# Kernel tuning notes

Measured on AMD Instinct MI355X. Metric: run time of the kernel, lower is better.

The kernel has to match this reference:

```python
import jax, jax.numpy as jnp
import numpy as np

DIM_GATE = 256
DIM_BIAS = 128
H = 8
D = 32
EPS = 1e-5


def _layernorm(t, gamma, beta):
    mu = jnp.mean(t, axis=-1, keepdims=True)
    var = jnp.mean(jnp.square(t - mu), axis=-1, keepdims=True)
    return (t - mu) * jax.lax.rsqrt(var + EPS) * gamma + beta


def setup_inputs() -> dict:
    key = jax.random.key(0)
    ks = jax.random.split(key, 12)
    b, l = 2, 512
    x = jax.random.normal(ks[0], (b, l, DIM_GATE), dtype=jnp.float32)
    bias = jax.random.normal(ks[1], (b, l, l, DIM_BIAS), dtype=jnp.float32)
    s_g = 1.0 / np.sqrt(DIM_GATE)
    s_b = 1.0 / np.sqrt(DIM_BIAS)
    return {
        "x": x,
        "bias": bias,
        "g_gamma": jnp.ones((DIM_GATE,), jnp.float32),
        "g_beta": jnp.zeros((DIM_GATE,), jnp.float32),
        "b_gamma": jnp.ones((DIM_BIAS,), jnp.float32),
        "b_beta": jnp.zeros((DIM_BIAS,), jnp.float32),
        "Wq": jax.random.normal(ks[2], (DIM_GATE, H * D), jnp.float32) * s_g,
        "Wk": jax.random.normal(ks[3], (DIM_GATE, H * D), jnp.float32) * s_g,
        "Wv": jax.random.normal(ks[4], (DIM_GATE, H * D), jnp.float32) * s_g,
        "Wb": jax.random.normal(ks[5], (DIM_BIAS, H), jnp.float32) * s_b,
        "Wg": jax.random.normal(ks[6], (DIM_GATE, H * D), jnp.float32) * s_g,
        "bg": jnp.zeros((H * D,), jnp.float32),
        "Wout": jax.random.normal(ks[7], (H * D, DIM_GATE), jnp.float32) * s_g,
        "bout": jnp.zeros((DIM_GATE,), jnp.float32),
    }


def reference(x, bias, g_gamma, g_beta, b_gamma, b_beta, Wq, Wk, Wv, Wb, Wg, bg, Wout, bout):
    b, l, _ = x.shape
    scaling = 1.0 / np.sqrt(D)
    xn = _layernorm(x, g_gamma, g_beta)                      # [b,l,dg]
    bn = _layernorm(bias, b_gamma, b_beta)                   # [b,l,l,db]
    q = (xn @ Wq).reshape(b, l, H, D)                        # [b,l,h,d]
    k = (xn @ Wk).reshape(b, l, H, D) * scaling
    v = (xn @ Wv).reshape(b, l, H, D)
    pair_b = bn @ Wb                                         # [b,q,k,h]
    gate = jax.nn.sigmoid(xn @ Wg + bg)                      # [b,l,h*d]
    attn = jnp.einsum('bqhd,bkhd->bqkh', q, k) + pair_b      # [b,q,k,h]
    attn = jax.nn.softmax(attn, axis=-2)                     # softmax over k
    out = jnp.einsum('bqkh,bkhd->bqhd', attn, v).reshape(b, l, H * D)
    out = gate * out
    return out @ Wout + bout
```

## Files before the change

### kernel.cpp

```cpp
#include <hip/hip_runtime.h>
#include <math.h>

#define LSEQ 512
#define DG 256
#define DB 128
#define NH 8
#define HD 32
#define EPSV 1e-5f
#define LP2 516

typedef __attribute__((ext_vector_type(8))) short bf16x8;
typedef __attribute__((ext_vector_type(4))) float f32x4;

__device__ __forceinline__ unsigned short f2bf(float x) {
    unsigned int u = __float_as_uint(x);
    u += 0x7FFFu + ((u >> 16) & 1u);
    return (unsigned short)(u >> 16);
}
__device__ __forceinline__ float bf2f(unsigned short h) {
    return __uint_as_float(((unsigned int)h) << 16);
}

__global__ __launch_bounds__(256) void prep_pairb_kernel(
    const float* __restrict__ x, const float* __restrict__ g_gamma,
    const float* __restrict__ g_beta, const float* __restrict__ Wq,
    const float* __restrict__ Wk, const float* __restrict__ Wv,
    const float* __restrict__ Wg, const float* __restrict__ bg,
    float* __restrict__ q_ws, float* __restrict__ k_ws,
    float* __restrict__ v_ws, float* __restrict__ g_ws,
    const float* __restrict__ bias, const float* __restrict__ b_gamma,
    const float* __restrict__ b_beta, const float* __restrict__ Wb,
    float* __restrict__ pair_ws)
{
    __shared__ float lds[4 * 2 * 2048];
    const int t = threadIdx.x;

    if (blockIdx.x < 256) {
        float (*xs)[DG] = (float(*)[DG])lds;
        const int wave = t >> 6, lane = t & 63;
        const int row0 = blockIdx.x << 2;

        {
            const int row = row0 + wave;
            const float4 xv = *(const float4*)(x + (size_t)row * DG + lane * 4);
            float s  = xv.x + xv.y + xv.z + xv.w;
            float ss = xv.x*xv.x + xv.y*xv.y + xv.z*xv.z + xv.w*xv.w;
            #pragma unroll
            for (int m = 32; m >= 1; m >>= 1) { s += __shfl_xor(s, m); ss += __shfl_xor(ss, m); }
            const float mean = s * (1.f / DG);
            const float rstd = rsqrtf(ss * (1.f / DG) - mean * mean + EPSV);
            const float4 gg = *(const float4*)(g_gamma + lane * 4);
            const float4 gb = *(const float4*)(g_beta + lane * 4);
            float4 xo;
            xo.x = (xv.x - mean) * rstd * gg.x + gb.x;
            xo.y = (xv.y - mean) * rstd * gg.y + gb.y;
            xo.z = (xv.z - mean) * rstd * gg.z + gb.z;
            xo.w = (xv.w - mean) * rstd * gg.w + gb.w;
            *(float4*)&xs[wave][lane * 4] = xo;
        }
        __syncthreads();

        float aq[4] = {0,0,0,0}, ak[4] = {0,0,0,0}, av[4] = {0,0,0,0}, ag[4] = {0,0,0,0};
        #pragma unroll 4
        for (int c = 0; c < DG; ++c) {
            const float wq = Wq[(size_t)c * DG + t];
            const float wk = Wk[(size_t)c * DG + t];
            const float wv = Wv[(size_t)c * DG + t];
            const float wg = Wg[(size_t)c * DG + t];
            #pragma unroll
            for (int r = 0; r < 4; ++r) {
                const float xr = xs[r][c];
                aq[r] = fmaf(xr, wq, aq[r]);
                ak[r] = fmaf(xr, wk, ak[r]);
                av[r] = fmaf(xr, wv, av[r]);
                ag[r] = fmaf(xr, wg, ag[r]);
            }
        }

        const float scal = 0.17677669529663687f;
        const float bgv = bg[t];
        #pragma unroll
        for (int r = 0; r < 4; ++r) {
            const size_t o = (size_t)(row0 + r) * DG + t;
            q_ws[o] = aq[r];
            k_ws[o] = ak[r] * scal;
            v_ws[o] = av[r];
            g_ws[o] = 1.f / (1.f + __expf(-(ag[r] + bgv)));
        }
        return;
    }

    const int w = t >> 6, l = t & 63;
    const int n = l & 15, quad = l >> 4;
    const int bq = blockIdx.x - 256;

    bf16x8 gwhi[4], gwlo[4];
    float S1 = 0.f, S0 = 0.f;
    #pragma unroll
    for (int ks = 0; ks < 4; ++ks) {
        #pragma unroll
        for (int j = 0; j < 8; ++j) {
            const int c = ks * 32 + quad * 8 + j;
            const float wb = (n < 8) ? Wb[c * 8 + n] : 0.f;
            const float wv = b_gamma[c] * wb;
            S1 += wv;
            S0 += b_beta[c] * wb;
            unsigned short hi = f2bf(wv);
            unsigned short lo = f2bf(wv - bf2f(hi));
            if (n == 8) { hi = 0x3F80; lo = 0; }
            gwhi[ks][j] = (short)hi;
            gwlo[ks][j] = (short)lo;
        }
    }
    S1 += __shfl_xor(S1, 16); S1 += __shfl_xor(S1, 32);
    S0 += __shfl_xor(S0, 16); S0 += __shfl_xor(S0, 32);

    float* myl = lds + w * 4096;
    const size_t rowbase = (size_t)bq * LSEQ + w * 16;

    auto stage = [&](int tt, int buf) {
        const float* src = bias + (rowbase + (size_t)tt * 64) * DB;
        float* dst = myl + buf * 2048;
        #pragma unroll
        for (int i = 0; i < 8; ++i) {
            __builtin_amdgcn_global_load_lds(
                (const __attribute__((address_space(1))) void*)(src + i * 256 + l * 4),
                (__attribute__((address_space(3))) void*)(dst + i * 256 + l * 4),
                16, 0, 0);
        }
    };

    auto compute = [&](int tt, int buf) {
        const float* d = myl + buf * 2048 + n * 128 + quad * 8;
        f32x4 acc = {0.f, 0.f, 0.f, 0.f};
        float ssq = 0.f;
        #pragma unroll
        for (int ks = 0; ks < 4; ++ks) {
            const float4 x0 = *(const float4*)(d + ks * 32);
            const float4 x1 = *(const float4*)(d + ks * 32 + 4);
            ssq = fmaf(x0.x,x0.x, fmaf(x0.y,x0.y, fmaf(x0.z,x0.z, fmaf(x0.w,x0.w, ssq))));
            ssq = fmaf(x1.x,x1.x, fmaf(x1.y,x1.y, fmaf(x1.z,x1.z, fmaf(x1.w,x1.w, ssq))));
            const float xsv[8] = {x0.x,x0.y,x0.z,x0.w,x1.x,x1.y,x1.z,x1.w};
            bf16x8 ahi, alo;
            #pragma unroll
            for (int j = 0; j < 8; ++j) {
                const unsigned short hi = f2bf(xsv[j]);
                ahi[j] = (short)hi;
                alo[j] = (short)f2bf(xsv[j] - bf2f(hi));
            }
            acc = __builtin_amdgcn_mfma_f32_16x16x32_bf16(ahi, gwhi[ks], acc, 0, 0, 0);
            acc = __builtin_amdgcn_mfma_f32_16x16x32_bf16(alo, gwhi[ks], acc, 0, 0, 0);
            acc = __builtin_amdgcn_mfma_f32_16x16x32_bf16(ahi, gwlo[ks], acc, 0, 0, 0);
        }
        ssq += __shfl_xor(ssq, 16);
        ssq += __shfl_xor(ssq, 32);
        float* pout = pair_ws + (rowbase + (size_t)tt * 64 + quad * 4) * NH + n;
        #pragma unroll
        for (int reg = 0; reg < 4; ++reg) {
            const float sumr = __uint_as_float((unsigned)__builtin_amdgcn_ds_bpermute(
                (quad * 16 + 8) * 4, (int)__float_as_uint(acc[reg])));
            const float ssqr = __uint_as_float((unsigned)__builtin_amdgcn_ds_bpermute(
                (quad * 4 + reg) * 4, (int)__float_as_uint(ssq)));
            const float mean = sumr * (1.f / DB);
            const float var  = ssqr * (1.f / DB) - mean * mean;
            const float rstd = rsqrtf(var + EPSV);
            const float p = rstd * (acc[reg] - mean * S1) + S0;
            if (n < NH) pout[reg * NH] = p;
        }
    };

    stage(0, 0);
    stage(1, 1);
    asm volatile("s_waitcnt vmcnt(8)" ::: "memory");
    compute(0, 0);
    for (int tt = 1; tt < 7; ++tt) {
        stage(tt + 1, (tt + 1) & 1);
        asm volatile("s_waitcnt vmcnt(12)" ::: "memory");
        compute(tt, tt & 1);
    }
    asm volatile("s_waitcnt vmcnt(4)" ::: "memory");
    compute(7, 1);
}

__global__ __launch_bounds__(512) void attn_kernel(
    const float* __restrict__ pair_ws, const float* __restrict__ Wout,
    const float* __restrict__ bout, const float* __restrict__ q_ws,
    const float* __restrict__ k_ws, const float* __restrict__ v_ws,
    const float* __restrict__ g_ws, float* __restrict__ out)
{
    __shared__ float lg[2 * NH * LP2];
    __shared__ float q_s[2 * DG];
    __shared__ float ps[4 * 2 * 64 * 4];
    __shared__ float row_s[2 * DG];
    __shared__ float rden[16];

    const int t = threadIdx.x;
    const int b = blockIdx.x >> 8;
    const int q0 = (blockIdx.x & 255) * 2;

    {
        const float* pbase = pair_ws + ((size_t)(b * LSEQ + q0)) * LSEQ * NH;
        #pragma unroll
        for (int r = 0; r < 4; ++r) {
            const int f = r * 512 + t;
            const float4 pv = *(const float4*)(pbase + (size_t)f * 4);
            const int q = f >> 10;
            const int o = (f * 4) & 4095;
            const int k = o >> 3, hb = o & 7;
            float* dst = lg + (q * NH + hb) * LP2 + k;
            dst[0] = pv.x; dst[LP2] = pv.y; dst[2*LP2] = pv.z; dst[3*LP2] = pv.w;
        }
        q_s[t] = q_ws[((size_t)(b * LSEQ + q0)) * DG + t];
    }
    __syncthreads();

    {
        const int h = t >> 6;
        const int lane = t & 63;
        const int d4 = lane >> 3, r = lane & 7;
        const float4 qa = *(const float4*)(q_s + h * HD + d4 * 4);
        const float4 qb = *(const float4*)(q_s + DG + h * HD + d4 * 4);
        const float* kbase = k_ws + ((size_t)(b * LSEQ)) * DG + h * HD + d4 * 4;
        float* l0 = lg + (0 * NH + h) * LP2;
        float* l1 = lg + (1 * NH + h) * LP2;
        #pragma unroll 4
        for (int kb8 = 0; kb8 < 64; ++kb8) {
            const int krow = kb8 * 8 + r;
            const float4 kv = *(const float4*)(kbase + (size_t)krow * DG);
            float a0 = fmaf(kv.x, qa.x, fmaf(kv.y, qa.y, fmaf(kv.z, qa.z, kv.w * qa.w)));
            float a1 = fmaf(kv.x, qb.x, fmaf(kv.y, qb.y, fmaf(kv.z, qb.z, kv.w * qb.w)));
            a0 += __shfl_xor(a0, 8);  a1 += __shfl_xor(a1, 8);
            a0 += __shfl_xor(a0, 16); a1 += __shfl_xor(a1, 16);
            a0 += __shfl_xor(a0, 32); a1 += __shfl_xor(a1, 32);
            if (d4 == 0) { l0[krow] += a0; l1[krow] += a1; }
        }
    }
    __syncthreads();

    {
        const int qh = t >> 5, l32 = t & 31;
        float* lrow = lg + qh * LP2;
        float mx = -1e30f;
        #pragma unroll
        for (int i = 0; i < 16; ++i) mx = fmaxf(mx, lrow[l32 + i * 32]);
        #pragma unroll
        for (int m = 16; m >= 1; m >>= 1) mx = fmaxf(mx, __shfl_xor(mx, m));
        float s = 0.f;
        #pragma unroll
        for (int i = 0; i < 16; ++i) {
            const int k = l32 + i * 32;
            const float e = __expf(lrow[k] - mx);
            lrow[k] = e;
            s += e;
        }
        #pragma unroll
        for (int m = 16; m >= 1; m >>= 1) s += __shfl_xor(s, m);
        if (l32 == 0) rden[qh] = 1.f / s;
    }
    __syncthreads();

    {
        const int q = t >> 8, s4 = (t >> 6) & 3, c4 = t & 63;
        const int h = c4 >> 3;
        const float* vb = v_ws + ((size_t)(b * LSEQ + s4 * 128)) * DG + c4 * 4;
        const float* prow = lg + (q * NH + h) * LP2 + s4 * 128;
        float4 a = {0.f, 0.f, 0.f, 0.f};
        #pragma unroll 4
        for (int i = 0; i < 128; ++i) {
            const float p = prow[i];
            const float4 vv = *(const float4*)(vb + (size_t)i * DG);
            a.x = fmaf(p, vv.x, a.x);
            a.y = fmaf(p, vv.y, a.y);
            a.z = fmaf(p, vv.z, a.z);
            a.w = fmaf(p, vv.w, a.w);
        }
        *(float4*)&ps[((s4 * 2 + q) * 64 + c4) * 4] = a;
    }
    __syncthreads();
    if (t < 128) {
        const int q = t >> 6, c4 = t & 63, h = c4 >> 3;
        float4 a = *(const float4*)&ps[((0 * 2 + q) * 64 + c4) * 4];
        #pragma unroll
        for (int s4 = 1; s4 < 4; ++s4) {
            const float4 p4 = *(const float4*)&ps[((s4 * 2 + q) * 64 + c4) * 4];
            a.x += p4.x; a.y += p4.y; a.z += p4.z; a.w += p4.w;
        }
        const float sc = rden[q * NH + h];
        const float4 g4 = *(const float4*)(g_ws + ((size_t)(b * LSEQ + q0 + q)) * DG + c4 * 4);
        float* rs = row_s + q * DG + c4 * 4;
        rs[0] = a.x * sc * g4.x;
        rs[1] = a.y * sc * g4.y;
        rs[2] = a.z * sc * g4.z;
        rs[3] = a.w * sc * g4.w;
    }
    __syncthreads();

    {
        const int q = t >> 8, co = t & 255;
        const float* rs = row_s + q * DG;
        const float* wo = Wout + co;
        float a = 0.f;
        #pragma unroll 4
        for (int c = 0; c < DG; ++c)
            a = fmaf(rs[c], wo[(size_t)c * DG], a);
        out[((size_t)(b * LSEQ + q0 + q)) * DG + co] = a + bout[co];
    }
}

extern "C" void kernel_launch(void* const* d_in, const int* in_sizes, int n_in,
                              void* d_out, int out_size, void* d_ws, size_t ws_size,
                              hipStream_t stream)
{
    const float* x       = (const float*)d_in[0];
    const float* bias    = (const float*)d_in[1];
    const float* g_gamma = (const float*)d_in[2];
    const float* g_beta  = (const float*)d_in[3];
    const float* b_gamma = (const float*)d_in[4];
    const float* b_beta  = (const float*)d_in[5];
    const float* Wq      = (const float*)d_in[6];
    const float* Wk      = (const float*)d_in[7];
    const float* Wv      = (const float*)d_in[8];
    const float* Wb      = (const float*)d_in[9];
    const float* Wg      = (const float*)d_in[10];
    const float* bg      = (const float*)d_in[11];
    const float* Wout    = (const float*)d_in[12];
    const float* bout    = (const float*)d_in[13];
    float* out = (float*)d_out;

    float* ws      = (float*)d_ws;
    float* q_ws    = ws;
    float* k_ws    = ws + 262144;
    float* v_ws    = ws + 2 * 262144;
    float* g_ws    = ws + 3 * 262144;
    float* pair_ws = ws + 4 * 262144;

    hipLaunchKernelGGL(prep_pairb_kernel, dim3(1280), dim3(256), 0, stream,
                       x, g_gamma, g_beta, Wq, Wk, Wv, Wg, bg,
                       q_ws, k_ws, v_ws, g_ws,
                       bias, b_gamma, b_beta, Wb, pair_ws);
    hipLaunchKernelGGL(attn_kernel, dim3(512), dim3(512), 0, stream,
                       pair_ws, Wout, bout, q_ws, k_ws, v_ws, g_ws, out);
}
```

Baseline: 473.3 us.

## Fuse pair-bias layernorm projection into attention kernel, one query row per block

Moves the pair-bias layernorm+projection out of the prep kernel and into the attention kernel, so each block computes its query row's bias logits directly into LDS instead of writing them to and reading them back from a global workspace. Bias staging grows to triple buffering and is issued before the QK dot products, so the bias loads overlap that work. The attention kernel now handles one query row per 256-thread block (1024 blocks) instead of two rows per 512-thread block. The trade-off is that the QK^T, PV and output projection work no longer shares K, V and Wout loads across two queries, and LDS use per block rises, which may lower occupancy.

```diff
diff --git a/kernel.cpp b/kernel.cpp
--- a/kernel.cpp
+++ b/kernel.cpp
@@ -21,78 +21,87 @@
     return __uint_as_float(((unsigned int)h) << 16);
 }
 
-__global__ __launch_bounds__(256) void prep_pairb_kernel(
+__global__ __launch_bounds__(256) void prep_kernel(
     const float* __restrict__ x, const float* __restrict__ g_gamma,
     const float* __restrict__ g_beta, const float* __restrict__ Wq,
     const float* __restrict__ Wk, const float* __restrict__ Wv,
     const float* __restrict__ Wg, const float* __restrict__ bg,
     float* __restrict__ q_ws, float* __restrict__ k_ws,
-    float* __restrict__ v_ws, float* __restrict__ g_ws,
+    float* __restrict__ v_ws, float* __restrict__ g_ws)
+{
+    __shared__ float xs[4][DG];
+    const int t = threadIdx.x;
+    const int wave = t >> 6, lane = t & 63;
+    const int row0 = blockIdx.x << 2;
+
+    {
+        const int row = row0 + wave;
+        const float4 xv = *(const float4*)(x + (size_t)row * DG + lane * 4);
+        float s  = xv.x + xv.y + xv.z + xv.w;
+        float ss = xv.x*xv.x + xv.y*xv.y + xv.z*xv.z + xv.w*xv.w;
+        #pragma unroll
+        for (int m = 32; m >= 1; m >>= 1) { s += __shfl_xor(s, m); ss += __shfl_xor(ss, m); }
+        const float mean = s * (1.f / DG);
+        const float rstd = rsqrtf(ss * (1.f / DG) - mean * mean + EPSV);
+        const float4 gg = *(const float4*)(g_gamma + lane * 4);
+        const float4 gb = *(const float4*)(g_beta + lane * 4);
+        float4 xo;
+        xo.x = (xv.x - mean) * rstd * gg.x + gb.x;
+        xo.y = (xv.y - mean) * rstd * gg.y + gb.y;
+        xo.z = (xv.z - mean) * rstd * gg.z + gb.z;
+        xo.w = (xv.w - mean) * rstd * gg.w + gb.w;
+        *(float4*)&xs[wave][lane * 4] = xo;
+    }
+    __syncthreads();
+
+    float aq[4] = {0,0,0,0}, ak[4] = {0,0,0,0}, av[4] = {0,0,0,0}, ag[4] = {0,0,0,0};
+    #pragma unroll 4
+    for (int c = 0; c < DG; ++c) {
+        const float wq = Wq[(size_t)c * DG + t];
+        const float wk = Wk[(size_t)c * DG + t];
+        const float wv = Wv[(size_t)c * DG + t];
+        const float wg = Wg[(size_t)c * DG + t];
+        #pragma unroll
+        for (int r = 0; r < 4; ++r) {
+            const float xr = xs[r][c];
+            aq[r] = fmaf(xr, wq, aq[r]);
+            ak[r] = fmaf(xr, wk, ak[r]);
+            av[r] = fmaf(xr, wv, av[r]);
+            ag[r] = fmaf(xr, wg, ag[r]);
+        }
+    }
+
+    const float scal = 0.17677669529663687f;
+    const float bgv = bg[t];
+    #pragma unroll
+    for (int r = 0; r < 4; ++r) {
+        const size_t o = (size_t)(row0 + r) * DG + t;
+        q_ws[o] = aq[r];
+        k_ws[o] = ak[r] * scal;
+        v_ws[o] = av[r];
+        g_ws[o] = 1.f / (1.f + __expf(-(ag[r] + bgv)));
+    }
+}
+
+__global__ __launch_bounds__(256) void fused_kernel(
     const float* __restrict__ bias, const float* __restrict__ b_gamma,
     const float* __restrict__ b_beta, const float* __restrict__ Wb,
-    float* __restrict__ pair_ws)
+    const float* __restrict__ Wout, const float* __restrict__ bout,
+    const float* __restrict__ q_ws, const float* __restrict__ k_ws,
+    const float* __restrict__ v_ws, const float* __restrict__ g_ws,
+    float* __restrict__ out)
 {
-    __shared__ float lds[4 * 2 * 2048];
+    __shared__ float stg[4 * 3 * 2048];
+    __shared__ float lg[NH * LP2];
+    __shared__ float ps[4 * 64 * 4];
+    __shared__ float row_s[DG];
+    __shared__ float rden[NH];
+
     const int t = threadIdx.x;
-
-    if (blockIdx.x < 256) {
-        float (*xs)[DG] = (float(*)[DG])lds;
-        const int wave = t >> 6, lane = t & 63;
-        const int row0 = blockIdx.x << 2;
-
-        {
-            const int row = row0 + wave;
-            const float4 xv = *(const float4*)(x + (size_t)row * DG + lane * 4);
-            float s  = xv.x + xv.y + xv.z + xv.w;
-            float ss = xv.x*xv.x + xv.y*xv.y + xv.z*xv.z + xv.w*xv.w;
-            #pragma unroll
-            for (int m = 32; m >= 1; m >>= 1) { s += __shfl_xor(s, m); ss += __shfl_xor(ss, m); }
-            const float mean = s * (1.f / DG);
-            const float rstd = rsqrtf(ss * (1.f / DG) - mean * mean + EPSV);
-            const float4 gg = *(const float4*)(g_gamma + lane * 4);
-            const float4 gb = *(const float4*)(g_beta + lane * 4);
-            float4 xo;
-            xo.x = (xv.x - mean) * rstd * gg.x + gb.x;
-            xo.y = (xv.y - mean) * rstd * gg.y + gb.y;
-            xo.z = (xv.z - mean) * rstd * gg.z + gb.z;
-            xo.w = (xv.w - mean) * rstd * gg.w + gb.w;
-            *(float4*)&xs[wave][lane * 4] = xo;
-        }
-        __syncthreads();
-
-        float aq[4] = {0,0,0,0}, ak[4] = {0,0,0,0}, av[4] = {0,0,0,0}, ag[4] = {0,0,0,0};
-        #pragma unroll 4
-        for (int c = 0; c < DG; ++c) {
-            const float wq = Wq[(size_t)c * DG + t];
-            const float wk = Wk[(size_t)c * DG + t];
-            const float wv = Wv[(size_t)c * DG + t];
-            const float wg = Wg[(size_t)c * DG + t];
-            #pragma unroll
-            for (int r = 0; r < 4; ++r) {
-                const float xr = xs[r][c];
-                aq[r] = fmaf(xr, wq, aq[r]);
-                ak[r] = fmaf(xr, wk, ak[r]);
-                av[r] = fmaf(xr, wv, av[r]);
-                ag[r] = fmaf(xr, wg, ag[r]);
-            }
-        }
-
-        const float scal = 0.17677669529663687f;
-        const float bgv = bg[t];
-        #pragma unroll
-        for (int r = 0; r < 4; ++r) {
-            const size_t o = (size_t)(row0 + r) * DG + t;
-            q_ws[o] = aq[r];
-            k_ws[o] = ak[r] * scal;
-            v_ws[o] = av[r];
-            g_ws[o] = 1.f / (1.f + __expf(-(ag[r] + bgv)));
-        }
-        return;
-    }
-
     const int w = t >> 6, l = t & 63;
     const int n = l & 15, quad = l >> 4;
-    const int bq = blockIdx.x - 256;
+    const int bq = blockIdx.x;
+    const int b = bq >> 9;
 
     bf16x8 gwhi[4], gwlo[4];
     float S1 = 0.f, S0 = 0.f;
@@ -115,12 +124,12 @@
     S1 += __shfl_xor(S1, 16); S1 += __shfl_xor(S1, 32);
     S0 += __shfl_xor(S0, 16); S0 += __shfl_xor(S0, 32);
 
-    float* myl = lds + w * 4096;
+    float* myl = stg + w * 6144;
     const size_t rowbase = (size_t)bq * LSEQ + w * 16;
 
-    auto stage = [&](int tt, int buf) {
+    auto stage = [&](int tt) {
         const float* src = bias + (rowbase + (size_t)tt * 64) * DB;
-        float* dst = myl + buf * 2048;
+        float* dst = myl + (tt % 3) * 2048;
         #pragma unroll
         for (int i = 0; i < 8; ++i) {
             __builtin_amdgcn_global_load_lds(
@@ -130,8 +139,8 @@
         }
     };
 
-    auto compute = [&](int tt, int buf) {
-        const float* d = myl + buf * 2048 + n * 128 + quad * 8;
+    auto compute = [&](int tt) {
+        const float* d = myl + (tt % 3) * 2048 + n * 128 + quad * 8;
         f32x4 acc = {0.f, 0.f, 0.f, 0.f};
         float ssq = 0.f;
         #pragma unroll
@@ -154,7 +163,7 @@
         }
         ssq += __shfl_xor(ssq, 16);
         ssq += __shfl_xor(ssq, 32);
-        float* pout = pair_ws + (rowbase + (size_t)tt * 64 + quad * 4) * NH + n;
+        float* pl = lg + n * LP2 + (w * 16 + tt * 64 + quad * 4);
         #pragma unroll
         for (int reg = 0; reg < 4; ++reg) {
             const float sumr = __uint_as_float((unsigned)__builtin_amdgcn_ds_bpermute(
@@ -165,74 +174,43 @@
             const float var  = ssqr * (1.f / DB) - mean * mean;
             const float rstd = rsqrtf(var + EPSV);
             const float p = rstd * (acc[reg] - mean * S1) + S0;
-            if (n < NH) pout[reg * NH] = p;
+            if (n < NH) pl[reg] += p;
         }
     };
 
-    stage(0, 0);
-    stage(1, 1);
-    asm volatile("s_waitcnt vmcnt(8)" ::: "memory");
-    compute(0, 0);
-    for (int tt = 1; tt < 7; ++tt) {
-        stage(tt + 1, (tt + 1) & 1);
-        asm volatile("s_waitcnt vmcnt(12)" ::: "memory");
-        compute(tt, tt & 1);
-    }
-    asm volatile("s_waitcnt vmcnt(4)" ::: "memory");
-    compute(7, 1);
-}
-
-__global__ __launch_bounds__(512) void attn_kernel(
-    const float* __restrict__ pair_ws, const float* __restrict__ Wout,
-    const float* __restrict__ bout, const float* __restrict__ q_ws,
-    const float* __restrict__ k_ws, const float* __restrict__ v_ws,
-    const float* __restrict__ g_ws, float* __restrict__ out)
-{
-    __shared__ float lg[2 * NH * LP2];
-    __shared__ float q_s[2 * DG];
-    __shared__ float ps[4 * 2 * 64 * 4];
-    __shared__ float row_s[2 * DG];
-    __shared__ float rden[16];
-
-    const int t = threadIdx.x;
-    const int b = blockIdx.x >> 8;
-    const int q0 = (blockIdx.x & 255) * 2;
-
-    {
-        const float* pbase = pair_ws + ((size_t)(b * LSEQ + q0)) * LSEQ * NH;
-        #pragma unroll
-        for (int r = 0; r < 4; ++r) {
-            const int f = r * 512 + t;
-            const float4 pv = *(const float4*)(pbase + (size_t)f * 4);
-            const int q = f >> 10;
-            const int o = (f * 4) & 4095;
-            const int k = o >> 3, hb = o & 7;
-            float* dst = lg + (q * NH + hb) * LP2 + k;
-            dst[0] = pv.x; dst[LP2] = pv.y; dst[2*LP2] = pv.z; dst[3*LP2] = pv.w;
-        }
-        q_s[t] = q_ws[((size_t)(b * LSEQ + q0)) * DG + t];
-    }
-    __syncthreads();
-
-    {
-        const int h = t >> 6;
-        const int lane = t & 63;
-        const int d4 = lane >> 3, r = lane & 7;
-        const float4 qa = *(const float4*)(q_s + h * HD + d4 * 4);
-        const float4 qb = *(const float4*)(q_s + DG + h * HD + d4 * 4);
-        const float* kbase = k_ws + ((size_t)(b * LSEQ)) * DG + h * HD + d4 * 4;
-        float* l0 = lg + (0 * NH + h) * LP2;
-        float* l1 = lg + (1 * NH + h) * LP2;
-        #pragma unroll 4
-        for (int kb8 = 0; kb8 < 64; ++kb8) {
-            const int krow = kb8 * 8 + r;
-            const float4 kv = *(const float4*)(kbase + (size_t)krow * DG);
-            float a0 = fmaf(kv.x, qa.x, fmaf(kv.y, qa.y, fmaf(kv.z, qa.z, kv.w * qa.w)));
-            float a1 = fmaf(kv.x, qb.x, fmaf(kv.y, qb.y, fmaf(kv.z, qb.z, kv.w * qb.w)));
-            a0 += __shfl_xor(a0, 8);  a1 += __shfl_xor(a1, 8);
-            a0 += __shfl_xor(a0, 16); a1 += __shfl_xor(a1, 16);
-            a0 += __shfl_xor(a0, 32); a1 += __shfl_xor(a1, 32);
-            if (d4 == 0) { l0[krow] += a0; l1[krow] += a1; }
+    stage(0); stage(1); stage(2);
+
+    {
+        const int d4 = l >> 3, r = l & 7;
+        #pragma unroll
+        for (int p = 0; p < 2; ++p) {
+            const int h = w * 2 + p;
+            const float4 qa = *(const float4*)(q_ws + (size_t)bq * DG + h * HD + d4 * 4);
+            const float* kbase = k_ws + ((size_t)(b * LSEQ)) * DG + h * HD + d4 * 4;
+            float* lrow = lg + h * LP2;
+            #pragma unroll 4
+            for (int kb8 = 0; kb8 < 64; ++kb8) {
+                const int krow = kb8 * 8 + r;
+                const float4 kv = *(const float4*)(kbase + (size_t)krow * DG);
+                float a0 = fmaf(kv.x, qa.x, fmaf(kv.y, qa.y, fmaf(kv.z, qa.z, kv.w * qa.w)));
+                a0 += __shfl_xor(a0, 8);
+                a0 += __shfl_xor(a0, 16);
+                a0 += __shfl_xor(a0, 32);
+                if (d4 == 0) lrow[krow] = a0;
+            }
+        }
+    }
+    __syncthreads();
+
+    #pragma unroll
+    for (int tt = 0; tt < 8; ++tt) {
+        if (tt <= 5)      asm volatile("s_waitcnt vmcnt(16)" ::: "memory");
+        else if (tt == 6) asm volatile("s_waitcnt vmcnt(8)"  ::: "memory");
+        else              asm volatile("s_waitcnt vmcnt(0)"  ::: "memory");
+        compute(tt);
+        if (tt + 3 < 8) {
+            asm volatile("s_waitcnt lgkmcnt(0)" ::: "memory");
+            stage(tt + 3);
         }
     }
     __syncthreads();
@@ -260,10 +238,10 @@
     __syncthreads();
 
     {
-        const int q = t >> 8, s4 = (t >> 6) & 3, c4 = t & 63;
+        const int s4 = t >> 6, c4 = t & 63;
         const int h = c4 >> 3;
         const float* vb = v_ws + ((size_t)(b * LSEQ + s4 * 128)) * DG + c4 * 4;
-        const float* prow = lg + (q * NH + h) * LP2 + s4 * 128;
+        const float* prow = lg + h * LP2 + s4 * 128;
         float4 a = {0.f, 0.f, 0.f, 0.f};
         #pragma unroll 4
         for (int i = 0; i < 128; ++i) {
@@ -274,20 +252,20 @@
             a.z = fmaf(p, vv.z, a.z);
             a.w = fmaf(p, vv.w, a.w);
         }
-        *(float4*)&ps[((s4 * 2 + q) * 64 + c4) * 4] = a;
-    }
-    __syncthreads();
-    if (t < 128) {
-        const int q = t >> 6, c4 = t & 63, h = c4 >> 3;
-        float4 a = *(const float4*)&ps[((0 * 2 + q) * 64 + c4) * 4];
+        *(float4*)&ps[(s4 * 64 + c4) * 4] = a;
+    }
+    __syncthreads();
+    if (t < 64) {
+        const int c4 = t, h = c4 >> 3;
+        float4 a = *(const float4*)&ps[(0 * 64 + c4) * 4];
         #pragma unroll
         for (int s4 = 1; s4 < 4; ++s4) {
-            const float4 p4 = *(const float4*)&ps[((s4 * 2 + q) * 64 + c4) * 4];
+            const float4 p4 = *(const float4*)&ps[(s4 * 64 + c4) * 4];
             a.x += p4.x; a.y += p4.y; a.z += p4.z; a.w += p4.w;
         }
-        const float sc = rden[q * NH + h];
-        const float4 g4 = *(const float4*)(g_ws + ((size_t)(b * LSEQ + q0 + q)) * DG + c4 * 4);
-        float* rs = row_s + q * DG + c4 * 4;
+        const float sc = rden[h];
+        const float4 g4 = *(const float4*)(g_ws + (size_t)bq * DG + c4 * 4);
+        float* rs = row_s + c4 * 4;
         rs[0] = a.x * sc * g4.x;
         rs[1] = a.y * sc * g4.y;
         rs[2] = a.z * sc * g4.z;
@@ -296,14 +274,13 @@
     __syncthreads();
 
     {
-        const int q = t >> 8, co = t & 255;
-        const float* rs = row_s + q * DG;
+        const int co = t;
         const float* wo = Wout + co;
         float a = 0.f;
         #pragma unroll 4
         for (int c = 0; c < DG; ++c)
-            a = fmaf(rs[c], wo[(size_t)c * DG], a);
-        out[((size_t)(b * LSEQ + q0 + q)) * DG + co] = a + bout[co];
+            a = fmaf(row_s[c], wo[(size_t)c * DG], a);
+        out[(size_t)bq * DG + co] = a + bout[co];
     }
 }
 
@@ -327,17 +304,16 @@
     const float* bout    = (const float*)d_in[13];
     float* out = (float*)d_out;
 
-    float* ws      = (float*)d_ws;
-    float* q_ws    = ws;
-    float* k_ws    = ws + 262144;
-    float* v_ws    = ws + 2 * 262144;
-    float* g_ws    = ws + 3 * 262144;
-    float* pair_ws = ws + 4 * 262144;
-
-    hipLaunchKernelGGL(prep_pairb_kernel, dim3(1280), dim3(256), 0, stream,
+    float* ws   = (float*)d_ws;
+    float* q_ws = ws;
+    float* k_ws = ws + 262144;
+    float* v_ws = ws + 2 * 262144;
+    float* g_ws = ws + 3 * 262144;
+
+    hipLaunchKernelGGL(prep_kernel, dim3(256), dim3(256), 0, stream,
                        x, g_gamma, g_beta, Wq, Wk, Wv, Wg, bg,
-                       q_ws, k_ws, v_ws, g_ws,
-                       bias, b_gamma, b_beta, Wb, pair_ws);
-    hipLaunchKernelGGL(attn_kernel, dim3(512), dim3(512), 0, stream,
-                       pair_ws, Wout, bout, q_ws, k_ws, v_ws, g_ws, out);
-}
+                       q_ws, k_ws, v_ws, g_ws);
+    hipLaunchKernelGGL(fused_kernel, dim3(1024), dim3(256), 0, stream,
+                       bias, b_gamma, b_beta, Wb, Wout, bout,
+                       q_ws, k_ws, v_ws, g_ws, out);
+}
```

After: 726.9 us. +53.6%, slower.
